# Optimization experiments

Hardware: AMD Instinct MI355X
Metric: run time of the kernel (lower is better)

The kernel has to match this reference:

```python
import jax, jax.numpy as jnp
import numpy as np

B, S, E, H, D = 4, 2048, 2048, 16, 128
EPS = 1e-6


def _rope_cache(seq_len, dim, base=10000.0):
    # standard rotary cache, half-split layout matching rotate_half
    inv_freq = 1.0 / (base ** (np.arange(0, dim // 2, dtype=np.float32) / (dim // 2)))
    t = np.arange(seq_len, dtype=np.float32)
    freqs = np.outer(t, inv_freq)                     # [S, D/2]
    emb = np.concatenate([freqs, freqs], axis=-1)     # [S, D]
    cos = jnp.asarray(np.cos(emb))[None, :, None, :]  # [1, S, 1, D]
    sin = jnp.asarray(np.sin(emb))[None, :, None, :]
    return cos, sin


def setup_inputs() -> dict:
    key = jax.random.key(0)
    ks = jax.random.split(key, 5)
    scale = 1.0 / np.sqrt(E)
    x = jax.random.normal(ks[0], (B, S, E), dtype=jnp.float32)
    Wq = jax.random.normal(ks[1], (E, E), dtype=jnp.float32) * scale
    Wk = jax.random.normal(ks[2], (E, E), dtype=jnp.float32) * scale
    Wv = jax.random.normal(ks[3], (E, E), dtype=jnp.float32) * scale
    Wo = jax.random.normal(ks[4], (E, E), dtype=jnp.float32) * scale
    cos, sin = _rope_cache(S, D)
    return {"x": x, "cos": cos, "sin": sin, "Wq": Wq, "Wk": Wk, "Wv": Wv, "Wo": Wo}


def _rotate_half(t):
    d = t.shape[-1] // 2
    return jnp.concatenate([-t[..., d:], t[..., :d]], axis=-1)


def _rms_norm(t, eps):
    return t * jax.lax.rsqrt(jnp.mean(t * t, axis=-1, keepdims=True) + eps)


def reference(x, cos, sin, Wq, Wk, Wv, Wo):
    b, s, _ = x.shape
    # QKV projections (Linear without bias: x @ W.T), reshape to heads
    q = (x @ Wq.T).reshape(b, s, H, D)
    k = (x @ Wk.T).reshape(b, s, H, D)
    v = (x @ Wv.T).reshape(b, s, H, D)
    # RoPE then QK RMSNorm (no learned scale)
    q = _rms_norm(q * cos + _rotate_half(q) * sin, EPS)
    k = _rms_norm(k * cos + _rotate_half(k) * sin, EPS)
    # non-causal SDPA
    scores = jnp.einsum("bqhd,bkhd->bhqk", q, k) / np.sqrt(D)
    probs = jax.nn.softmax(scores, axis=-1)
    y = jnp.einsum("bhqk,bkhd->bqhd", probs, v).reshape(b, s, H * D)
    return y @ Wo.T
```

## Files before the change

### kernel.cpp

```cpp
#include <hip/hip_runtime.h>
#include <hip/hip_bf16.h>
#include <math.h>


typedef __bf16 bf16_t;
typedef __bf16 bf16x2 __attribute__((ext_vector_type(2)));
typedef __bf16 bf16x4 __attribute__((ext_vector_type(4)));
typedef __bf16 bf16x8 __attribute__((ext_vector_type(8)));
typedef float f32x2 __attribute__((ext_vector_type(2)));
typedef float f32x4 __attribute__((ext_vector_type(4)));
typedef float f32x16 __attribute__((ext_vector_type(16)));
typedef unsigned int u32;
typedef u32 u32x4 __attribute__((ext_vector_type(4)));

typedef __attribute__((address_space(1))) const void gas_cvoid;
typedef __attribute__((address_space(3))) void las_void;

#define MFMA16(a, b, c) __builtin_amdgcn_mfma_f32_16x16x32_bf16((a), (b), (c), 0, 0, 0)
#define MFMA32(a, b, c) __builtin_amdgcn_mfma_f32_32x32x16_bf16((a), (b), (c), 0, 0, 0)

__device__ __forceinline__ void gload16(const void* g, void* l) {
  __builtin_amdgcn_global_load_lds((gas_cvoid*)g, (las_void*)l, 16, 0, 0);
}
__device__ __forceinline__ void pl32(u32& a, u32& b) {
  asm volatile("v_permlane32_swap_b32 %0, %1" : "+v"(a), "+v"(b));
}

__global__ __launch_bounds__(256) void cvt_bf16(const float* __restrict__ in,
                                                bf16_t* __restrict__ out) {
  const size_t i = ((size_t)blockIdx.x * 256 + threadIdx.x) * 4;
  f32x4 v = *(const f32x4*)&in[i];
  bf16x4 o;
#pragma unroll
  for (int j = 0; j < 4; ++j) o[j] = (bf16_t)v[j];
  *(bf16x4*)&out[i] = o;
}
__global__ __launch_bounds__(256) void cvt_w4(const float* __restrict__ w0,
                                              const float* __restrict__ w1,
                                              const float* __restrict__ w2,
                                              const float* __restrict__ w3,
                                              bf16_t* __restrict__ o0,
                                              bf16_t* __restrict__ o1,
                                              bf16_t* __restrict__ o2,
                                              bf16_t* __restrict__ o3) {
  const int which = blockIdx.x >> 12;
  const float* in = which == 0 ? w0 : which == 1 ? w1 : which == 2 ? w2 : w3;
  bf16_t* out = which == 0 ? o0 : which == 1 ? o1 : which == 2 ? o2 : o3;
  const size_t i = ((size_t)(blockIdx.x & 4095) * 256 + threadIdx.x) * 4;
  f32x4 v = *(const f32x4*)&in[i];
  bf16x4 o;
#pragma unroll
  for (int j = 0; j < 4; ++j) o[j] = (bf16_t)v[j];
  *(bf16x4*)&out[i] = o;
}

template <int MODE, typename CT, int NT_T>
__global__ __launch_bounds__(512, 2) void gemm8(const bf16_t* __restrict__ A,
                                                const bf16_t* __restrict__ Bt,
                                                CT* __restrict__ C) {
  constexpr int K = 2048;
  __shared__ __attribute__((aligned(16))) char lds[131072];
  const int tid = threadIdx.x;
  const int wave = tid >> 6, lane = tid & 63;
  const int bid = blockIdx.x;
  const int swz = (bid & 7) * 32 + (bid >> 3);
  const int m0 = (swz / NT_T) * 256, n0 = (swz % NT_T) * 256;

  const int srow = tid >> 3;
  const int scol = ((tid & 7) ^ (srow & 7)) * 8;
  const bf16_t* aBase = A + (size_t)(m0 + srow) * K + scol;
  const bf16_t* bBase = Bt + (size_t)(n0 + srow) * K + scol;

  const int wm = wave >> 2, wn = wave & 3;
  const int l15 = lane & 15, l4 = lane >> 4;
  const int axor = l15 & 7;

  f32x4 acc[8][4] = {};

  auto stageA = [&](int tt, int nbuf) {
#pragma unroll
    for (int h = 0; h < 2; ++h)
#pragma unroll
      for (int cc = 0; cc < 2; ++cc)
        gload16(aBase + (size_t)(h * 128 + cc * 64) * K + tt * 64,
                lds + nbuf * 65536 + h * 16384 + cc * 8192 + wave * 1024);
  };
  auto stageB = [&](int tt, int nbuf) {
#pragma unroll
    for (int h = 0; h < 2; ++h)
#pragma unroll
      for (int cc = 0; cc < 2; ++cc)
        gload16(bBase + (size_t)(h * 128 + cc * 64) * K + tt * 64,
                lds + nbuf * 65536 + 32768 + h * 16384 + cc * 8192 + wave * 1024);
  };

  stageA(0, 0);
  stageB(0, 0);
  __syncthreads();

  for (int t = 0; t < 32; ++t) {
    const int buf = t & 1, nbuf = buf ^ 1;
    const char* la = lds + buf * 65536 + wm * 16384;
    const char* lb = lds + buf * 65536 + 32768 + (wn >> 1) * 16384 + (wn & 1) * 8192;
    bf16x8 bF[4][2];
#pragma unroll
    for (int q = 0; q < 4; ++q) {
      bf16x8 aF[2][2];
#pragma unroll
      for (int dm = 0; dm < 2; ++dm)
#pragma unroll
        for (int kk = 0; kk < 2; ++kk)
          aF[dm][kk] = *(const bf16x8*)(la + ((q * 2 + dm) * 16 + l15) * 128 +
                                        ((kk * 4 + l4) ^ axor) * 16);
      if (q == 0) {
#pragma unroll
        for (int ni = 0; ni < 4; ++ni)
#pragma unroll
          for (int kk = 0; kk < 2; ++kk)
            bF[ni][kk] = *(const bf16x8*)(lb + (ni * 16 + l15) * 128 +
                                          ((kk * 4 + l4) ^ axor) * 16);
        if (t < 31) stageA(t + 1, nbuf);
      }
      if (q == 1 && t < 31) stageB(t + 1, nbuf);
      __builtin_amdgcn_s_barrier();
      __builtin_amdgcn_s_setprio(1);
#pragma unroll
      for (int kk = 0; kk < 2; ++kk)
#pragma unroll
        for (int dm = 0; dm < 2; ++dm)
#pragma unroll
          for (int ni = 0; ni < 4; ++ni)
            acc[q * 2 + dm][ni] = MFMA16(aF[dm][kk], bF[ni][kk], acc[q * 2 + dm][ni]);
      __builtin_amdgcn_s_setprio(0);
      if (q < 3)
        __builtin_amdgcn_s_barrier();
      else
        __syncthreads();
    }
  }

  const int rBase = m0 + wm * 128 + l4 * 4;
  const int cBase = n0 + wn * 64 + l15;
#pragma unroll
  for (int mi = 0; mi < 8; ++mi)
#pragma unroll
    for (int ni = 0; ni < 4; ++ni)
#pragma unroll
      for (int j = 0; j < 4; ++j) {
        const int r = rBase + mi * 16 + j;
        const int c = cBase + ni * 16;
        const CT v = (CT)acc[mi][ni][j];
        if (MODE == 0) {
          const int b = r >> 11, s = r & 2047, hh = c >> 7, d = c & 127;
          C[(((size_t)(b * 16 + hh)) * 2048 + s) * 128 + d] = v;
        } else if (MODE == 1) {
          C[(size_t)r * 2048 + c] = v;
        } else {
          const int hh = r >> 7, dd = r & 127, b = c >> 11, s = c & 2047;
          C[((size_t)(b * 16 + hh) * 128 + dd) * 2048 + s] = v;
        }
      }
}

__global__ __launch_bounds__(256) void rope_rms(bf16_t* __restrict__ T,
                                                const float* __restrict__ Cs,
                                                const float* __restrict__ Sn) {
  const int wave = threadIdx.x >> 6, lane = threadIdx.x & 63;
#pragma unroll 1
  for (int rr = 0; rr < 8; ++rr) {
    const size_t row = (size_t)blockIdx.x * 32 + wave * 8 + rr;
    const int s = (int)(row & 2047);
    bf16_t* p = &T[row * 128 + 2 * lane];
    const float a0 = (float)p[0], a1 = (float)p[1];
    f32x2 cv = *(const f32x2*)&Cs[(size_t)s * 128 + 2 * lane];
    f32x2 sv = *(const f32x2*)&Sn[(size_t)s * 128 + 2 * lane];
    const float p0 = __shfl_xor(a0, 32);
    const float p1 = __shfl_xor(a1, 32);
    const float sg = (lane < 32) ? -1.f : 1.f;
    const float r0 = a0 * cv.x + sg * p0 * sv.x;
    const float r1 = a1 * cv.y + sg * p1 * sv.y;
    float ss = r0 * r0 + r1 * r1;
#pragma unroll
    for (int off = 1; off < 64; off <<= 1) ss += __shfl_xor(ss, off);
    const float inv = rsqrtf(ss * (1.0f / 128.0f) + 1e-6f);
    p[0] = (bf16_t)(r0 * inv);
    p[1] = (bf16_t)(r1 * inv);
  }
}

__global__ __launch_bounds__(512, 2) void attn_fwd(const bf16_t* __restrict__ Q,
                                                   const bf16_t* __restrict__ K,
                                                   const bf16_t* __restrict__ Vt,
                                                   bf16_t* __restrict__ Y) {
  __shared__ __attribute__((aligned(16))) bf16_t ldsK[2][64 * 128];
  __shared__ __attribute__((aligned(16))) bf16_t ldsV[2][128 * 64];
  const int tid = threadIdx.x, wave = tid >> 6, lane = tid & 63;
  const int l31 = lane & 31, hi = lane >> 5;
  const int pid = blockIdx.x;
  const int bh = (pid & 7) * 8 + ((pid >> 3) & 7);
  const int qb = pid >> 6;
  const int b = bh >> 4, h = bh & 15;
  const bf16_t* Qh = Q + (size_t)bh * 2048 * 128;
  const bf16_t* Kh = K + (size_t)bh * 2048 * 128;
  const bf16_t* Vh = Vt + (size_t)bh * 128 * 2048;
  const int q0 = qb * 256 + wave * 32;

  bf16x8 qf[8];
#pragma unroll
  for (int dk = 0; dk < 8; ++dk)
    qf[dk] = *(const bf16x8*)&Qh[(size_t)(q0 + l31) * 128 + dk * 16 + hi * 8];

  f32x16 ot[4] = {};
  float m_r = -1e30f, l_r = 0.f;
  const float scale = 0.08838834764831845f;

  auto stage = [&](int kt, int bu) {
#pragma unroll
    for (int i = 0; i < 2; ++i) {
      const int G = wave * 64 + lane + i * 512;
      char* dstK = (char*)&ldsK[bu][0] + (wave * 64 + i * 512) * 16;
      char* dstV = (char*)&ldsV[bu][0] + (wave * 64 + i * 512) * 16;
      const int kvr = G >> 4, glk = G & 15;
      gload16(Kh + (size_t)(kt * 64 + kvr) * 128 + ((glk ^ (kvr & 7)) * 8), dstK);
      const int dr = G >> 3, glv = G & 7;
      gload16(Vh + (size_t)dr * 2048 + kt * 64 + ((glv ^ (dr & 7)) * 8), dstV);
    }
  };

  stage(0, 0);
  stage(1, 1);
  asm volatile("s_waitcnt vmcnt(4)" ::: "memory");
  __builtin_amdgcn_s_barrier();
  __builtin_amdgcn_sched_barrier(0);

  for (int kt = 0; kt < 32; ++kt) {
    const int bu = kt & 1;

    f32x16 sa0 = {}, sa1 = {};
    const int r7 = l31 & 7;
    __builtin_amdgcn_s_setprio(1);
#pragma unroll
    for (int dk = 0; dk < 8; ++dk) {
      const int g = ((dk << 1) | hi) ^ r7;
      bf16x8 kf0 = *(const bf16x8*)&ldsK[bu][l31 * 128 + g * 8];
      bf16x8 kf1 = *(const bf16x8*)&ldsK[bu][(32 + l31) * 128 + g * 8];
      sa0 = MFMA32(kf0, qf[dk], sa0);
      sa1 = MFMA32(kf1, qf[dk], sa1);
    }
    __builtin_amdgcn_s_setprio(0);

    float tm[16];
#pragma unroll
    for (int j = 0; j < 16; ++j) tm[j] = fmaxf(sa0[j], sa1[j]);
#pragma unroll
    for (int s = 8; s; s >>= 1)
#pragma unroll
      for (int j = 0; j < s; ++j) tm[j] = fmaxf(tm[j], tm[j + s]);
    float mx = fmaxf(tm[0], __shfl_xor(tm[0], 32)) * scale;
    if (__any(mx > m_r + 8.f)) {
      const float mn = fmaxf(m_r, mx);
      const float corr = __expf(m_r - mn);
      m_r = mn;
      l_r *= corr;
#pragma unroll
      for (int db = 0; db < 4; ++db)
#pragma unroll
        for (int j = 0; j < 16; ++j) ot[db][j] *= corr;
    }
    u32 w[2][8];
    float ssum = 0.f;
#pragma unroll
    for (int i = 0; i < 8; ++i) {
      const float p0 = __expf(sa0[2 * i] * scale - m_r);
      const float p1 = __expf(sa0[2 * i + 1] * scale - m_r);
      const float p2 = __expf(sa1[2 * i] * scale - m_r);
      const float p3 = __expf(sa1[2 * i + 1] * scale - m_r);
      ssum += (p0 + p1) + (p2 + p3);
      bf16x2 t0, t1;
      t0[0] = (bf16_t)p0; t0[1] = (bf16_t)p1;
      t1[0] = (bf16_t)p2; t1[1] = (bf16_t)p3;
      w[0][i] = __builtin_bit_cast(u32, t0);
      w[1][i] = __builtin_bit_cast(u32, t1);
    }
    ssum += __shfl_xor(ssum, 32);
    l_r += ssum;

#pragma unroll
    for (int ks = 0; ks < 4; ++ks) {
      const int tsel = ks >> 1, k4 = (ks & 1) * 4;
      u32 a0 = w[tsel][k4 + 0], b0 = w[tsel][k4 + 2];
      u32 a1 = w[tsel][k4 + 1], b1 = w[tsel][k4 + 3];
      pl32(a0, b0);
      pl32(a1, b1);
      u32x4 fw;
      fw.x = a0; fw.y = a1; fw.z = b0; fw.w = b1;
      const bf16x8 pf = __builtin_bit_cast(bf16x8, fw);
      const int gv = ((ks << 1) | hi) ^ r7;
      __builtin_amdgcn_s_setprio(1);
#pragma unroll
      for (int db = 0; db < 4; ++db) {
        bf16x8 vf = *(const bf16x8*)&ldsV[bu][(db * 32 + l31) * 64 + gv * 8];
        ot[db] = MFMA32(vf, pf, ot[db]);
      }
      __builtin_amdgcn_s_setprio(0);
    }

    __builtin_amdgcn_s_barrier();
    __builtin_amdgcn_sched_barrier(0);
    if (kt < 30) {
      stage(kt + 2, bu);
      asm volatile("s_waitcnt vmcnt(4)" ::: "memory");
    } else {
      asm volatile("s_waitcnt vmcnt(0)" ::: "memory");
    }
    __builtin_amdgcn_s_barrier();
    __builtin_amdgcn_sched_barrier(0);
  }

  const float rl = 1.f / l_r;
  const size_t yrow = ((size_t)(b * 2048 + q0 + l31) * 16 + h) * 128;
#pragma unroll
  for (int db = 0; db < 4; ++db)
#pragma unroll
    for (int g2 = 0; g2 < 4; ++g2) {
      bf16x4 ov;
#pragma unroll
      for (int j = 0; j < 4; ++j) ov[j] = (bf16_t)(ot[db][g2 * 4 + j] * rl);
      *(bf16x4*)&Y[yrow + db * 32 + g2 * 8 + hi * 4] = ov;
    }
}

extern "C" void kernel_launch(void* const* d_in, const int* in_sizes, int n_in,
                              void* d_out, int out_size, void* d_ws, size_t ws_size,
                              hipStream_t stream) {
  const float* x = (const float*)d_in[0];
  const float* cs = (const float*)d_in[1];
  const float* sn = (const float*)d_in[2];
  const float* Wq = (const float*)d_in[3];
  const float* Wk = (const float*)d_in[4];
  const float* Wv = (const float*)d_in[5];
  const float* Wo = (const float*)d_in[6];

  bf16_t* ws = (bf16_t*)d_ws;
  const size_t TSZ = (size_t)4 * 2048 * 2048;
  const size_t WSZ = (size_t)2048 * 2048;
  bf16_t* xb = ws;
  bf16_t* Wqb = ws + TSZ;
  bf16_t* Wkb = Wqb + WSZ;
  bf16_t* Wvb = Wkb + WSZ;
  bf16_t* Wob = Wvb + WSZ;
  bf16_t* Qb = ws + 2 * TSZ;
  bf16_t* Kb = Qb + TSZ;
  bf16_t* Vtb = Kb + TSZ;
  bf16_t* Yb = xb;

  cvt_bf16<<<16384, 256, 0, stream>>>(x, xb);
  cvt_w4<<<16384, 256, 0, stream>>>(Wq, Wk, Wv, Wo, Wqb, Wkb, Wvb, Wob);

  gemm8<0, bf16_t, 8><<<256, 512, 0, stream>>>(xb, Wqb, Qb);
  gemm8<0, bf16_t, 8><<<256, 512, 0, stream>>>(xb, Wkb, Kb);
  gemm8<2, bf16_t, 32><<<256, 512, 0, stream>>>(Wvb, xb, Vtb);
  rope_rms<<<4096, 256, 0, stream>>>(Qb, cs, sn);
  rope_rms<<<4096, 256, 0, stream>>>(Kb, cs, sn);
  attn_fwd<<<512, 512, 0, stream>>>(Qb, Kb, Vtb, Yb);
  gemm8<1, float, 8><<<256, 512, 0, stream>>>(Yb, Wob, (float*)d_out);
}
```

Measured before the change: 489.0 us.

## Split GEMM prefetch across sub-steps with vmcnt waits and re-swizzle attention LDS

The GEMM main loop now spreads the next tile's global-to-LDS loads over the four sub-iterations, two loads per step. Each step waits with explicit vmcnt counts and a single barrier instead of a full __syncthreads at the end of each K tile, so loads stay in flight behind the MFMAs. The attention kernel changes its K/V LDS XOR swizzle to mix row-group bits into the key, meant to cut LDS bank conflicts on the fragment reads. The partial vmcnt waits depend on exact load ordering and could race if the count is wrong.

```diff
diff --git a/kernel.cpp b/kernel.cpp
--- a/kernel.cpp
+++ b/kernel.cpp
@@ -74,37 +74,38 @@
   const int wm = wave >> 2, wn = wave & 3;
   const int l15 = lane & 15, l4 = lane >> 4;
   const int axor = l15 & 7;
+  char* const wdst = lds + wave * 1024;
 
   f32x4 acc[8][4] = {};
 
-  auto stageA = [&](int tt, int nbuf) {
-#pragma unroll
-    for (int h = 0; h < 2; ++h)
-#pragma unroll
-      for (int cc = 0; cc < 2; ++cc)
-        gload16(aBase + (size_t)(h * 128 + cc * 64) * K + tt * 64,
-                lds + nbuf * 65536 + h * 16384 + cc * 8192 + wave * 1024);
-  };
-  auto stageB = [&](int tt, int nbuf) {
-#pragma unroll
-    for (int h = 0; h < 2; ++h)
-#pragma unroll
-      for (int cc = 0; cc < 2; ++cc)
-        gload16(bBase + (size_t)(h * 128 + cc * 64) * K + tt * 64,
-                lds + nbuf * 65536 + 32768 + h * 16384 + cc * 8192 + wave * 1024);
-  };
-
-  stageA(0, 0);
-  stageB(0, 0);
-  __syncthreads();
+  gload16(bBase, wdst + 32768);
+  gload16(bBase + (size_t)64 * K, wdst + 32768 + 8192);
+  gload16(bBase + (size_t)128 * K, wdst + 32768 + 16384);
+  gload16(bBase + (size_t)192 * K, wdst + 32768 + 24576);
+  gload16(aBase, wdst);
+  gload16(aBase + (size_t)128 * K, wdst + 16384);
+  gload16(aBase + (size_t)64 * K, wdst + 8192);
+  gload16(aBase + (size_t)192 * K, wdst + 24576);
 
   for (int t = 0; t < 32; ++t) {
     const int buf = t & 1, nbuf = buf ^ 1;
     const char* la = lds + buf * 65536 + wm * 16384;
     const char* lb = lds + buf * 65536 + 32768 + (wn >> 1) * 16384 + (wn & 1) * 8192;
+    char* const ndst = wdst + nbuf * 65536;
     bf16x8 bF[4][2];
 #pragma unroll
     for (int q = 0; q < 4; ++q) {
+      if (q == 0) {
+        asm volatile("s_waitcnt vmcnt(2)" ::: "memory");
+      } else if (q == 2) {
+        if (t < 31)
+          asm volatile("s_waitcnt vmcnt(4)" ::: "memory");
+        else
+          asm volatile("s_waitcnt vmcnt(0)" ::: "memory");
+      }
+      __builtin_amdgcn_s_barrier();
+      __builtin_amdgcn_sched_barrier(0);
+
       bf16x8 aF[2][2];
 #pragma unroll
       for (int dm = 0; dm < 2; ++dm)
@@ -119,10 +120,23 @@
           for (int kk = 0; kk < 2; ++kk)
             bF[ni][kk] = *(const bf16x8*)(lb + (ni * 16 + l15) * 128 +
                                           ((kk * 4 + l4) ^ axor) * 16);
-        if (t < 31) stageA(t + 1, nbuf);
-      }
-      if (q == 1 && t < 31) stageB(t + 1, nbuf);
-      __builtin_amdgcn_s_barrier();
+      }
+      if (t < 31) {
+        const int off = (t + 1) * 64;
+        if (q == 0) {
+          gload16(bBase + off, ndst + 32768);
+          gload16(bBase + (size_t)64 * K + off, ndst + 32768 + 8192);
+        } else if (q == 1) {
+          gload16(bBase + (size_t)128 * K + off, ndst + 32768 + 16384);
+          gload16(bBase + (size_t)192 * K + off, ndst + 32768 + 24576);
+        } else if (q == 2) {
+          gload16(aBase + off, ndst);
+          gload16(aBase + (size_t)128 * K + off, ndst + 16384);
+        } else {
+          gload16(aBase + (size_t)64 * K + off, ndst + 8192);
+          gload16(aBase + (size_t)192 * K + off, ndst + 24576);
+        }
+      }
       __builtin_amdgcn_s_setprio(1);
 #pragma unroll
       for (int kk = 0; kk < 2; ++kk)
@@ -132,10 +146,6 @@
           for (int ni = 0; ni < 4; ++ni)
             acc[q * 2 + dm][ni] = MFMA16(aF[dm][kk], bF[ni][kk], acc[q * 2 + dm][ni]);
       __builtin_amdgcn_s_setprio(0);
-      if (q < 3)
-        __builtin_amdgcn_s_barrier();
-      else
-        __syncthreads();
     }
   }
 
@@ -214,6 +224,9 @@
   float m_r = -1e30f, l_r = 0.f;
   const float scale = 0.08838834764831845f;
 
+  const int vb = ((l31 & 7) + (l31 >> 3)) & 7;
+  const int vb4 = (vb + 4) & 7;
+
   auto stage = [&](int kt, int bu) {
 #pragma unroll
     for (int i = 0; i < 2; ++i) {
@@ -221,9 +234,11 @@
       char* dstK = (char*)&ldsK[bu][0] + (wave * 64 + i * 512) * 16;
       char* dstV = (char*)&ldsV[bu][0] + (wave * 64 + i * 512) * 16;
       const int kvr = G >> 4, glk = G & 15;
-      gload16(Kh + (size_t)(kt * 64 + kvr) * 128 + ((glk ^ (kvr & 7)) * 8), dstK);
+      const int vk = ((kvr & 7) + (kvr >> 3)) & 7;
+      gload16(Kh + (size_t)(kt * 64 + kvr) * 128 + ((glk ^ vk) * 8), dstK);
       const int dr = G >> 3, glv = G & 7;
-      gload16(Vh + (size_t)dr * 2048 + kt * 64 + ((glv ^ (dr & 7)) * 8), dstV);
+      const int vv = ((dr & 7) + (dr >> 3)) & 7;
+      gload16(Vh + (size_t)dr * 2048 + kt * 64 + ((glv ^ vv) * 8), dstV);
     }
   };
 
@@ -237,13 +252,12 @@
     const int bu = kt & 1;
 
     f32x16 sa0 = {}, sa1 = {};
-    const int r7 = l31 & 7;
     __builtin_amdgcn_s_setprio(1);
 #pragma unroll
     for (int dk = 0; dk < 8; ++dk) {
-      const int g = ((dk << 1) | hi) ^ r7;
-      bf16x8 kf0 = *(const bf16x8*)&ldsK[bu][l31 * 128 + g * 8];
-      bf16x8 kf1 = *(const bf16x8*)&ldsK[bu][(32 + l31) * 128 + g * 8];
+      const int gbase = (dk << 1) | hi;
+      bf16x8 kf0 = *(const bf16x8*)&ldsK[bu][l31 * 128 + (gbase ^ vb) * 8];
+      bf16x8 kf1 = *(const bf16x8*)&ldsK[bu][(32 + l31) * 128 + (gbase ^ vb4) * 8];
       sa0 = MFMA32(kf0, qf[dk], sa0);
       sa1 = MFMA32(kf1, qf[dk], sa1);
     }
@@ -295,11 +309,12 @@
       u32x4 fw;
       fw.x = a0; fw.y = a1; fw.z = b0; fw.w = b1;
       const bf16x8 pf = __builtin_bit_cast(bf16x8, fw);
-      const int gv = ((ks << 1) | hi) ^ r7;
+      const int gvb = (ks << 1) | hi;
       __builtin_amdgcn_s_setprio(1);
 #pragma unroll
       for (int db = 0; db < 4; ++db) {
-        bf16x8 vf = *(const bf16x8*)&ldsV[bu][(db * 32 + l31) * 64 + gv * 8];
+        const int vmask = (db & 1) ? vb4 : vb;
+        bf16x8 vf = *(const bf16x8*)&ldsV[bu][(db * 32 + l31) * 64 + (gvb ^ vmask) * 8];
         ot[db] = MFMA32(vf, pf, ot[db]);
       }
       __builtin_amdgcn_s_setprio(0);
```

After: 494.1 us. Within noise of the previous version (+1.1%).
